# Kernel tuning notes

Measured on AMD Instinct MI355X. Metric: run time of the kernel, lower is better.

## Reference

```python
import jax, jax.numpy as jnp
import numpy as np

FORGET_BIAS = 1.0  # tf.nn.rnn_cell.LSTMCell default


def _lstm_scan(x_btE, W, b, hidden):
    """x: (B,T,E). W: (E+H, 4H), gate order i, j, f, o (TF LSTMCell)."""
    B = x_btE.shape[0]
    h0 = jnp.zeros((B, hidden), x_btE.dtype)
    c0 = jnp.zeros((B, hidden), x_btE.dtype)

    def step(carry, x_t):
        h, c = carry
        z = jnp.concatenate([x_t, h], axis=-1) @ W + b  # (B, 4H)
        i, j, f, o = jnp.split(z, 4, axis=-1)
        c_new = jax.nn.sigmoid(f + FORGET_BIAS) * c + jax.nn.sigmoid(i) * jnp.tanh(j)
        h_new = jax.nn.sigmoid(o) * jnp.tanh(c_new)
        return (h_new, c_new), h_new

    (_, _), hs = jax.lax.scan(step, (h0, c0), jnp.swapaxes(x_btE, 0, 1))
    return jnp.swapaxes(hs, 0, 1)  # (B, T, H)


def setup_inputs() -> dict:
    key = jax.random.key(0)
    ks = jax.random.split(key, 5)
    B, T, V, E, H, C = 256, 120, 50000, 256, 1024, 5
    tokens = jax.random.randint(ks[0], (B, T, 1), 0, V, dtype=jnp.int32)
    embeddings = jax.random.normal(ks[1], (V, E), jnp.float32) * 0.1
    W_lstm = jax.random.normal(ks[2], (E + H, 4 * H), jnp.float32) * (1.0 / np.sqrt(E + H))
    b_lstm = jnp.zeros((4 * H,), jnp.float32)
    U = jax.random.normal(ks[3], (H, C), jnp.float32) * (1.0 / np.sqrt(H))
    b2 = jnp.zeros((C,), jnp.float32)
    return {"tokens": tokens, "embeddings": embeddings, "W_lstm": W_lstm,
            "b_lstm": b_lstm, "U": U, "b2": b2}


def reference(tokens, embeddings, W_lstm, b_lstm, U, b2):
    B, T, F = tokens.shape  # F == n_features == 1
    E = embeddings.shape[1]
    H = U.shape[0]
    # embedding lookup + reshape to (B, T, F*E)
    x = embeddings[tokens].reshape(B, T, F * E)
    outputs = _lstm_scan(x, W_lstm, b_lstm, H)  # (B, T, H); dropout keep_prob=1 -> identity
    preds = outputs.reshape(-1, H) @ U + b2
    return preds.reshape(B, T, -1)  # (B, max_length, n_classes)
```

## Files before the change

### kernel.cpp

```cpp
#include <hip/hip_runtime.h>

typedef unsigned short u16;
typedef unsigned int u32;
typedef unsigned long long u64;
typedef int   v4i  __attribute__((ext_vector_type(4)));
typedef short v8s  __attribute__((ext_vector_type(8)));
typedef float v2f  __attribute__((ext_vector_type(2)));
typedef float v16f __attribute__((ext_vector_type(16)));

#define B_ 256
#define T_ 120
#define E_ 256
#define H_ 1024
#define K_ 1280
#define LDH 1032
#define LDX 264

#define WS_WF   0
#define WS_X    10485760
#define WS_HS   26214400
#define WS_BAR  89128960

__device__ __forceinline__ u16 f2bf(float f) {
    union { float f; u32 u; } v; v.f = f;
    u32 r = v.u + 0x7fffu + ((v.u >> 16) & 1u);
    return (u16)(r >> 16);
}
__device__ __forceinline__ float bf2f(u16 u) {
    union { u32 u; float f; } v; v.u = ((u32)u) << 16; return v.f;
}
__device__ __forceinline__ float fsig(float x) {
    float t = __builtin_amdgcn_exp2f(-1.44269504f * x);
    return __builtin_amdgcn_rcpf(1.0f + t);
}
__device__ __forceinline__ float ftanh_(float x) {
    float xc = fminf(8.0f, fmaxf(-8.0f, x));
    float t = __builtin_amdgcn_exp2f(2.88539008f * xc);
    return (t - 1.0f) * __builtin_amdgcn_rcpf(t + 1.0f);
}

__global__ void prep_w(const float* __restrict__ W, u16* __restrict__ Wf) {
    int tg  = blockIdx.x * 256 + threadIdx.x;
    int l   = tg & 63;
    int fid = tg >> 6;
    int f   = fid % 40;
    int cid = fid / 40;
    int khalf = cid & 1;
    int g   = (cid >> 1) & 3;
    int nc  = cid >> 3;
    int s   = 2 * f + khalf;
    int kb  = s * 16 + ((l >> 5) << 3);
    int col = g * 1024 + nc * 32 + (l & 31);
    u16 o[8];
#pragma unroll
    for (int j = 0; j < 8; ++j)
        o[j] = f2bf(W[(size_t)(kb + j) * 4096 + col]);
    *(v4i*)(Wf + (((size_t)fid << 6) + l) * 8) = *(v4i*)o;
}

__global__ void prep_x(const int* __restrict__ tokens, const float* __restrict__ emb,
                       u16* __restrict__ X) {
    int v   = blockIdx.x * 256 + threadIdx.x;
    int e8  = v & 31;
    int row = v >> 5;
    int t = row >> 8, b = row & 255;
    int tok = tokens[b * T_ + t];
    const float* src = emb + (size_t)tok * E_ + e8 * 8;
    u16 o[8];
#pragma unroll
    for (int j = 0; j < 8; ++j) o[j] = f2bf(src[j]);
    *(v4i*)(X + (size_t)row * E_ + e8 * 8) = *(v4i*)o;
}

__global__ __launch_bounds__(512, 2) void lstm_main(
    const u16* __restrict__ Wf, const u16* __restrict__ X,
    const float* __restrict__ b_lstm, u16* __restrict__ hs,
    u32* __restrict__ bar) {

    __shared__ u16  hbuf[32 * LDH];
    __shared__ u16  xbuf[32 * LDX];
    __shared__ float gates[2 * 4 * 32 * 34];
    __shared__ float bias[128];

    const int tid   = threadIdx.x;
    const int lane  = tid & 63;
    const int wv    = tid >> 6;
    const int g     = wv >> 1;
    const int khalf = wv & 1;
    const int bid   = blockIdx.x;
    const int mchunk = bid & 7;
    const int nc    = bid >> 3;
    const int m0    = mchunk << 5;

    if (tid < 128) bias[tid] = b_lstm[(tid >> 5) * H_ + (nc << 5) + (tid & 31)];

    v8s Wr[40];
    {
        const int cid = nc * 8 + g * 2 + khalf;
        const v4i* wsrc = (const v4i*)(Wf + (size_t)cid * 40 * 512);
#pragma unroll
        for (int f = 0; f < 40; ++f)
            Wr[f] = __builtin_bit_cast(v8s, wsrc[f * 64 + lane]);
    }
#pragma unroll
    for (int f = 0; f < 40; ++f) asm volatile("" : "+v"(Wr[f]));

    {
        const v4i* xs = (const v4i*)(X + (size_t)m0 * E_);
#pragma unroll
        for (int i = 0; i < 2; ++i) {
            int idx = tid + i * 512;
            int r = idx >> 5, c8 = idx & 31;
            *(v4i*)&xbuf[r * LDX + c8 * 8] = xs[r * 32 + c8];
        }
    }
    __syncthreads();

    const u16* Ax = &xbuf[(lane & 31) * LDX + ((lane >> 5) << 3)];
    const u16* Ah = &hbuf[(lane & 31) * LDH + ((lane >> 5) << 3)];

    v16f acc = {0,0,0,0,0,0,0,0,0,0,0,0,0,0,0,0};
#pragma unroll
    for (int f = 0; f < 8; ++f) {
        v8s a = *(const v8s*)(Ax + (2 * f + khalf) * 16);
        acc = __builtin_amdgcn_mfma_f32_32x32x16_bf16(a, Wr[f], acc, 0, 0, 0);
    }

    float cst[2] = {0.f, 0.f};
    const int cm  = tid >> 4;
    const int cn2 = (tid & 15) << 1;
    u32* hs32 = (u32*)hs;

    for (int t = 0; t < T_; ++t) {
        if (t > 0) {
            if (tid == 0) {
                u32* p = &bar[mchunk * T_ + (t - 1)];
                while (__hip_atomic_load(p, __ATOMIC_RELAXED, __HIP_MEMORY_SCOPE_AGENT) < 32u)
                    __builtin_amdgcn_s_sleep(1);
            }
            __syncthreads();
            {
                const v4i* hsrc = (const v4i*)(hs + ((size_t)(t - 1) * B_ + m0) * H_);
#pragma unroll
                for (int i = 0; i < 8; ++i) {
                    int idx = tid + i * 512;
                    int r = idx >> 7, c = idx & 127;
                    *(v4i*)&hbuf[r * LDH + c * 8] = hsrc[r * 128 + c];
                }
            }
            __syncthreads();
#pragma unroll
            for (int f = 8; f < 40; ++f) {
                v8s a = *(const v8s*)(Ah + ((2 * f + khalf) * 16 - 256));
                acc = __builtin_amdgcn_mfma_f32_32x32x16_bf16(a, Wr[f], acc, 0, 0, 0);
            }
        }

        {
            float* gb = &gates[((khalf << 2) + g) * 1088];
            int col = lane & 31, rq = (lane >> 5) << 2;
#pragma unroll
            for (int reg = 0; reg < 16; ++reg) {
                int row = (reg & 3) + ((reg >> 2) << 3) + rq;
                gb[row * 34 + col] = acc[reg];
            }
        }
        __syncthreads();

        u32 hpack = 0;
        {
            v2f zz[4];
#pragma unroll
            for (int gg = 0; gg < 4; ++gg) {
                v2f a = *(const v2f*)&gates[gg * 1088 + cm * 34 + cn2];
                v2f b = *(const v2f*)&gates[(4 + gg) * 1088 + cm * 34 + cn2];
                zz[gg].x = a.x + b.x; zz[gg].y = a.y + b.y;
            }
#pragma unroll
            for (int q = 0; q < 2; ++q) {
                int n = cn2 + q;
                float ip = zz[0][q] + bias[n];
                float jp = zz[1][q] + bias[32 + n];
                float fp = zz[2][q] + bias[64 + n] + 1.0f;
                float op = zz[3][q] + bias[96 + n];
                float cc = fsig(fp) * cst[q] + fsig(ip) * ftanh_(jp);
                cst[q] = cc;
                hpack |= ((u32)f2bf(fsig(op) * ftanh_(cc))) << (16 * q);
            }
        }
        __hip_atomic_store(&hs32[((size_t)t * B_ + m0 + cm) * 512 + (nc << 4) + (tid & 15)],
                           hpack, __ATOMIC_RELAXED, __HIP_MEMORY_SCOPE_AGENT);

        if (t + 1 < T_) {
            {
                const v4i* xs = (const v4i*)(X + ((size_t)(t + 1) * B_ + m0) * E_);
#pragma unroll
                for (int i = 0; i < 2; ++i) {
                    int idx = tid + i * 512;
                    int r = idx >> 5, c8 = idx & 31;
                    *(v4i*)&xbuf[r * LDX + c8 * 8] = xs[r * 32 + c8];
                }
            }
            asm volatile("s_waitcnt vmcnt(0)" ::: "memory");
            __syncthreads();
            if (tid == 0)
                __hip_atomic_fetch_add(&bar[mchunk * T_ + t], 1u,
                                       __ATOMIC_RELAXED, __HIP_MEMORY_SCOPE_AGENT);
#pragma unroll
            for (int reg = 0; reg < 16; ++reg) acc[reg] = 0.f;
#pragma unroll
            for (int f = 0; f < 8; ++f) {
                v8s a = *(const v8s*)(Ax + (2 * f + khalf) * 16);
                acc = __builtin_amdgcn_mfma_f32_32x32x16_bf16(a, Wr[f], acc, 0, 0, 0);
            }
        }
    }
}

__global__ void proj_kernel(const u16* __restrict__ hs, const float* __restrict__ U,
                            const float* __restrict__ b2, float* __restrict__ out) {
    __shared__ float Ul[H_ * 5];
    int tid = threadIdx.x;
    for (int i = tid; i < H_ * 5; i += 256) Ul[i] = U[i];
    __syncthreads();
    int wv = tid >> 6, lane = tid & 63;
    int row = blockIdx.x * 4 + wv;
    int t = row >> 8, b = row & 255;
    const v4i* hp = (const v4i*)(hs + (size_t)row * H_);
    float p[5] = {0.f, 0.f, 0.f, 0.f, 0.f};
#pragma unroll
    for (int half = 0; half < 2; ++half) {
        v4i hv = hp[lane * 2 + half];
        u16 us[8];
        *(v4i*)us = hv;
#pragma unroll
        for (int j = 0; j < 8; ++j) {
            float hf = bf2f(us[j]);
            int k = lane * 16 + half * 8 + j;
#pragma unroll
            for (int c = 0; c < 5; ++c) p[c] += hf * Ul[k * 5 + c];
        }
    }
#pragma unroll
    for (int c = 0; c < 5; ++c)
        for (int off = 32; off > 0; off >>= 1)
            p[c] += __shfl_down(p[c], off, 64);
    if (lane == 0) {
#pragma unroll
        for (int c = 0; c < 5; ++c)
            out[((size_t)b * T_ + t) * 5 + c] = p[c] + b2[c];
    }
}

extern "C" void kernel_launch(void* const* d_in, const int* in_sizes, int n_in,
                              void* d_out, int out_size, void* d_ws, size_t ws_size,
                              hipStream_t stream) {
    const int*   tokens = (const int*)d_in[0];
    const float* emb    = (const float*)d_in[1];
    const float* W      = (const float*)d_in[2];
    const float* b_l    = (const float*)d_in[3];
    const float* U      = (const float*)d_in[4];
    const float* b2     = (const float*)d_in[5];
    float* out = (float*)d_out;

    char* ws = (char*)d_ws;
    u16* Wf  = (u16*)(ws + WS_WF);
    u16* X   = (u16*)(ws + WS_X);
    u16* hs  = (u16*)(ws + WS_HS);
    u32* bar = (u32*)(ws + WS_BAR);

    hipMemsetAsync(bar, 0, 8 * T_ * sizeof(u32), stream);
    prep_w<<<2560, 256, 0, stream>>>(W, Wf);
    prep_x<<<3840, 256, 0, stream>>>(tokens, emb, X);
    lstm_main<<<256, 512, 0, stream>>>(Wf, X, b_l, hs, bar);
    proj_kernel<<<7680, 256, 0, stream>>>(hs, U, b2, out);
}
```

Before: 668.6 us.

## Async h loads to LDS with split waits, coalesce W prep, batch projection rows

The recurrent h-state copy into LDS now uses global_load_lds direct-to-LDS loads. Completion is waited on in two halves so the first half of the hidden-part MFMAs can start before the second half of h has arrived. The next-step X prefetch is moved earlier, before the gate nonlinearities, to overlap its latency. prep_w now transposes through an LDS tile for coalesced reads, and proj_kernel processes 16 rows per wave so the U table is loaded into LDS far fewer times. The split vmcnt waits assume each wave's loads land in the expected half-rows, which is a correctness risk if the ordering assumptions are off.

```diff
diff --git a/kernel.cpp b/kernel.cpp
--- a/kernel.cpp
+++ b/kernel.cpp
@@ -38,24 +38,40 @@
     float t = __builtin_amdgcn_exp2f(2.88539008f * xc);
     return (t - 1.0f) * __builtin_amdgcn_rcpf(t + 1.0f);
 }
+__device__ __forceinline__ void gl_lds16(const void* g, void* l) {
+    __builtin_amdgcn_global_load_lds(
+        (const __attribute__((address_space(1))) void*)g,
+        (__attribute__((address_space(3))) void*)l, 16, 0, 0);
+}
 
 __global__ void prep_w(const float* __restrict__ W, u16* __restrict__ Wf) {
-    int tg  = blockIdx.x * 256 + threadIdx.x;
-    int l   = tg & 63;
-    int fid = tg >> 6;
-    int f   = fid % 40;
-    int cid = fid / 40;
-    int khalf = cid & 1;
-    int g   = (cid >> 1) & 3;
-    int nc  = cid >> 3;
-    int s   = 2 * f + khalf;
-    int kb  = s * 16 + ((l >> 5) << 3);
-    int col = g * 1024 + nc * 32 + (l & 31);
-    u16 o[8];
-#pragma unroll
-    for (int j = 0; j < 8; ++j)
-        o[j] = f2bf(W[(size_t)(kb + j) * 4096 + col]);
-    *(v4i*)(Wf + (((size_t)fid << 6) + l) * 8) = *(v4i*)o;
+    __shared__ u16 tile[32 * 136];
+    int bid = blockIdx.x;
+    int cid = bid / 5, fo = bid % 5;
+    int kh  = cid & 1, g = (cid >> 1) & 3, nc = cid >> 3;
+    int colbase = g * 1024 + nc * 32;
+    int tid = threadIdx.x;
+    int c = tid & 31, r = tid >> 5;
+
+#pragma unroll
+    for (int fl = 0; fl < 8; ++fl) {
+        int k0 = (2 * (fo * 8 + fl) + kh) * 16;
+#pragma unroll
+        for (int rr = 0; rr < 2; ++rr) {
+            int row = r + rr * 8;
+            float v = W[(size_t)(k0 + row) * 4096 + colbase + c];
+            tile[c * 136 + fl * 16 + row] = f2bf(v);
+        }
+    }
+    __syncthreads();
+
+    int lane = tid & 63;
+#pragma unroll
+    for (int pass = 0; pass < 2; ++pass) {
+        int fl = (tid >> 6) + pass * 4;
+        v4i o = *(const v4i*)&tile[(lane & 31) * 136 + fl * 16 + ((lane >> 5) << 3)];
+        *(v4i*)(Wf + (((size_t)(cid * 40 + fo * 8 + fl)) << 9) + lane * 8) = o;
+    }
 }
 
 __global__ void prep_x(const int* __restrict__ tokens, const float* __restrict__ emb,
@@ -140,17 +156,26 @@
             }
             __syncthreads();
             {
-                const v4i* hsrc = (const v4i*)(hs + ((size_t)(t - 1) * B_ + m0) * H_);
-#pragma unroll
-                for (int i = 0; i < 8; ++i) {
-                    int idx = tid + i * 512;
-                    int r = idx >> 7, c = idx & 127;
-                    *(v4i*)&hbuf[r * LDH + c * 8] = hsrc[r * 128 + c];
-                }
-            }
-            __syncthreads();
-#pragma unroll
-            for (int f = 8; f < 40; ++f) {
+                const u16* srcb = hs + ((size_t)(t - 1) * B_ + m0) * H_;
+                int r0 = wv << 2;
+#pragma unroll
+                for (int half = 0; half < 2; ++half)
+#pragma unroll
+                    for (int i = 0; i < 4; ++i) {
+                        int r = r0 + i;
+                        gl_lds16(srcb + (size_t)r * H_ + half * 512 + lane * 8,
+                                 &hbuf[r * LDH + half * 512]);
+                    }
+            }
+            asm volatile("s_waitcnt vmcnt(4)\n\ts_barrier" ::: "memory");
+#pragma unroll
+            for (int f = 8; f < 24; ++f) {
+                v8s a = *(const v8s*)(Ah + ((2 * f + khalf) * 16 - 256));
+                acc = __builtin_amdgcn_mfma_f32_32x32x16_bf16(a, Wr[f], acc, 0, 0, 0);
+            }
+            asm volatile("s_waitcnt vmcnt(0)\n\ts_barrier" ::: "memory");
+#pragma unroll
+            for (int f = 24; f < 40; ++f) {
                 v8s a = *(const v8s*)(Ah + ((2 * f + khalf) * 16 - 256));
                 acc = __builtin_amdgcn_mfma_f32_32x32x16_bf16(a, Wr[f], acc, 0, 0, 0);
             }
@@ -166,6 +191,16 @@
             }
         }
         __syncthreads();
+
+        if (t + 1 < T_) {
+            const v4i* xs = (const v4i*)(X + ((size_t)(t + 1) * B_ + m0) * E_);
+#pragma unroll
+            for (int i = 0; i < 2; ++i) {
+                int idx = tid + i * 512;
+                int r = idx >> 5, c8 = idx & 31;
+                *(v4i*)&xbuf[r * LDX + c8 * 8] = xs[r * 32 + c8];
+            }
+        }
 
         u32 hpack = 0;
         {
@@ -192,15 +227,6 @@
                            hpack, __ATOMIC_RELAXED, __HIP_MEMORY_SCOPE_AGENT);
 
         if (t + 1 < T_) {
-            {
-                const v4i* xs = (const v4i*)(X + ((size_t)(t + 1) * B_ + m0) * E_);
-#pragma unroll
-                for (int i = 0; i < 2; ++i) {
-                    int idx = tid + i * 512;
-                    int r = idx >> 5, c8 = idx & 31;
-                    *(v4i*)&xbuf[r * LDX + c8 * 8] = xs[r * 32 + c8];
-                }
-            }
             asm volatile("s_waitcnt vmcnt(0)" ::: "memory");
             __syncthreads();
             if (tid == 0)
@@ -224,31 +250,34 @@
     for (int i = tid; i < H_ * 5; i += 256) Ul[i] = U[i];
     __syncthreads();
     int wv = tid >> 6, lane = tid & 63;
-    int row = blockIdx.x * 4 + wv;
-    int t = row >> 8, b = row & 255;
-    const v4i* hp = (const v4i*)(hs + (size_t)row * H_);
-    float p[5] = {0.f, 0.f, 0.f, 0.f, 0.f};
-#pragma unroll
-    for (int half = 0; half < 2; ++half) {
-        v4i hv = hp[lane * 2 + half];
-        u16 us[8];
-        *(v4i*)us = hv;
-#pragma unroll
-        for (int j = 0; j < 8; ++j) {
-            float hf = bf2f(us[j]);
-            int k = lane * 16 + half * 8 + j;
-#pragma unroll
-            for (int c = 0; c < 5; ++c) p[c] += hf * Ul[k * 5 + c];
-        }
-    }
-#pragma unroll
-    for (int c = 0; c < 5; ++c)
-        for (int off = 32; off > 0; off >>= 1)
-            p[c] += __shfl_down(p[c], off, 64);
-    if (lane == 0) {
+#pragma unroll 1
+    for (int i = 0; i < 16; ++i) {
+        int row = blockIdx.x * 64 + wv * 16 + i;
+        int t = row >> 8, b = row & 255;
+        const v4i* hp = (const v4i*)(hs + (size_t)row * H_);
+        float p[5] = {0.f, 0.f, 0.f, 0.f, 0.f};
+#pragma unroll
+        for (int half = 0; half < 2; ++half) {
+            v4i hv = hp[lane * 2 + half];
+            u16 us[8];
+            *(v4i*)us = hv;
+#pragma unroll
+            for (int j = 0; j < 8; ++j) {
+                float hf = bf2f(us[j]);
+                int k = lane * 16 + half * 8 + j;
+#pragma unroll
+                for (int c = 0; c < 5; ++c) p[c] += hf * Ul[k * 5 + c];
+            }
+        }
 #pragma unroll
         for (int c = 0; c < 5; ++c)
-            out[((size_t)b * T_ + t) * 5 + c] = p[c] + b2[c];
+            for (int off = 32; off > 0; off >>= 1)
+                p[c] += __shfl_down(p[c], off, 64);
+        if (lane == 0) {
+#pragma unroll
+            for (int c = 0; c < 5; ++c)
+                out[((size_t)b * T_ + t) * 5 + c] = p[c] + b2[c];
+        }
     }
 }
 
@@ -270,8 +299,8 @@
     u32* bar = (u32*)(ws + WS_BAR);
 
     hipMemsetAsync(bar, 0, 8 * T_ * sizeof(u32), stream);
-    prep_w<<<2560, 256, 0, stream>>>(W, Wf);
+    prep_w<<<1280, 256, 0, stream>>>(W, Wf);
     prep_x<<<3840, 256, 0, stream>>>(tokens, emb, X);
     lstm_main<<<256, 512, 0, stream>>>(Wf, X, b_l, hs, bar);
-    proj_kernel<<<7680, 256, 0, stream>>>(hs, U, b2, out);
-}
+    proj_kernel<<<480, 256, 0, stream>>>(hs, U, b2, out);
+}
```

Measured after the change: 607.9 us. 9.1% less time.
